# Kernel optimization log

Measured on AMD Instinct MI355X. Metric: run time of the kernel, lower is better.

The kernel has to match this reference:

```python
import jax, jax.numpy as jnp
import numpy as np

N_NODES = 100000
N_PER_GRAPH = 200
N_GRAPHS = N_NODES // N_PER_GRAPH
N_EDGES = 400000
F_IN = 37
H = 128          # node_hidden == transformer_hidden == fc_hidden
HEADS = 8
K_SEEDS = 75     # ceil(0.25 * 300) -> PyG GMT defaults


def _lin(key, out_d, in_d):
    kw, kb = jax.random.split(key)
    w = jax.random.normal(kw, (out_d, in_d), jnp.float32) * float(1.0 / np.sqrt(in_d))
    b = jax.random.normal(kb, (out_d,), jnp.float32) * 0.02
    return w, b


def gcn_layer(x, W, b, src, dst, n):
    # PyG GCNConv with add_self_loops and symmetric deg^-1/2 normalization
    h = x @ W.T                                   # [n, out]
    deg = jnp.ones((n,), h.dtype).at[dst].add(1.0)   # in-degree + self loop
    dinv = jax.lax.rsqrt(deg)
    msg = h[src] * (dinv[src] * dinv[dst])[:, None]  # gather + edge normalize
    agg = jnp.zeros_like(h).at[dst].add(msg)         # scatter-add
    agg = agg + h * (dinv * dinv)[:, None]           # self-loop message
    return agg + b


def attn_block(Q, K, V, fo_W, fo_b):
    # MAB core of GMT: multi-head attention (scaled by sqrt(dim_V)) + rFF residual
    B, nq, d = Q.shape
    dh = d // HEADS
    Qh = Q.reshape(B, nq, HEADS, dh)
    Kh = K.reshape(B, K.shape[1], HEADS, dh)
    Vh = V.reshape(B, V.shape[1], HEADS, dh)
    scores = jnp.einsum('bqhd,bkhd->bhqk', Qh, Kh) / jnp.sqrt(jnp.asarray(d, Q.dtype))
    A = jax.nn.softmax(scores, axis=-1)
    O = jnp.einsum('bhqk,bkhd->bqhd', A, Vh).reshape(B, nq, d)
    out = Q + O
    return out + jax.nn.relu(out @ fo_W.T + fo_b)


def setup_inputs() -> dict:
    key = jax.random.key(0)
    k = iter(jax.random.split(key, 64))
    inp = {}
    inp['herg_em'] = jax.random.normal(next(k), (1, 1280), jnp.float32)
    inp['x'] = jax.random.normal(next(k), (N_NODES, F_IN), jnp.float32)
    inp['edge_attr'] = jax.random.normal(next(k), (N_EDGES, 4), jnp.float32)
    inp['mol_rep'] = jax.random.normal(next(k), (N_GRAPHS, 11), jnp.float32)
    for i, in_d in enumerate([F_IN, H, H, H]):
        inp[f'conv_W{i}'], inp[f'conv_b{i}'] = _lin(next(k), H, in_d)
    inp['lin1_W'], inp['lin1_b'] = _lin(next(k), H, H)
    inp['lin2_W'], inp['lin2_b'] = _lin(next(k), H, H)
    inp['S1'] = jax.random.normal(next(k), (1, K_SEEDS, H), jnp.float32) * 0.1
    for p in ['pma1', 'sab', 'pma2']:
        for nm in ['fq', 'k', 'v', 'fo']:
            inp[f'{p}_{nm}_W'], inp[f'{p}_{nm}_b'] = _lin(next(k), H, H)
    inp['S2'] = jax.random.normal(next(k), (1, 1, H), jnp.float32) * 0.1
    inp['herg_lin_W'], inp['herg_lin_b'] = _lin(next(k), H, 1280)
    inp['herg_out_W'], inp['herg_out_b'] = _lin(next(k), H, 2 * H)
    inp['fc0_W'], inp['fc0_b'] = _lin(next(k), H, H)
    inp['sig_W'], inp['sig_b'] = _lin(next(k), 1, H)
    inp['edge_index'] = jax.random.randint(next(k), (2, N_EDGES), 0, N_NODES, dtype=jnp.int32)
    inp['batch'] = jnp.arange(N_NODES, dtype=jnp.int32) // N_PER_GRAPH
    return inp


def reference(herg_em, x, edge_attr, mol_rep,
              conv_W0, conv_b0, conv_W1, conv_b1, conv_W2, conv_b2, conv_W3, conv_b3,
              lin1_W, lin1_b, lin2_W, lin2_b,
              S1, pma1_fq_W, pma1_fq_b, pma1_k_W, pma1_k_b, pma1_v_W, pma1_v_b, pma1_fo_W, pma1_fo_b,
              sab_fq_W, sab_fq_b, sab_k_W, sab_k_b, sab_v_W, sab_v_b, sab_fo_W, sab_fo_b,
              S2, pma2_fq_W, pma2_fq_b, pma2_k_W, pma2_k_b, pma2_v_W, pma2_v_b, pma2_fo_W, pma2_fo_b,
              herg_lin_W, herg_lin_b, herg_out_W, herg_out_b,
              fc0_W, fc0_b, sig_W, sig_b,
              edge_index, batch):
    src, dst = edge_index[0], edge_index[1]
    n = x.shape[0]

    # stacked GCNConv + ReLU
    h = jax.nn.relu(gcn_layer(x, conv_W0, conv_b0, src, dst, n))
    for W, b in ((conv_W1, conv_b1), (conv_W2, conv_b2), (conv_W3, conv_b3)):
        h = jax.nn.relu(gcn_layer(h, W, b, src, dst, n))

    # GraphMultisetTransformer: lin1 -> GMPool_G -> SelfAtt -> GMPool_I -> lin2
    hx = h @ lin1_W.T + lin1_b                     # [N, H]
    B = N_GRAPHS

    # GMPool_G: seeds attend to GCNConv-projected keys/values (dense per graph)
    Q = jnp.broadcast_to(S1, (B, K_SEEDS, H)) @ pma1_fq_W.T + pma1_fq_b
    K = gcn_layer(hx, pma1_k_W, pma1_k_b, src, dst, n).reshape(B, N_PER_GRAPH, H)
    V = gcn_layer(hx, pma1_v_W, pma1_v_b, src, dst, n).reshape(B, N_PER_GRAPH, H)
    xb = attn_block(Q, K, V, pma1_fo_W, pma1_fo_b)     # [B, 75, H]

    # SelfAtt (SAB)
    Q = xb @ sab_fq_W.T + sab_fq_b
    K = xb @ sab_k_W.T + sab_k_b
    V = xb @ sab_v_W.T + sab_v_b
    xb = attn_block(Q, K, V, sab_fo_W, sab_fo_b)       # [B, 75, H]

    # GMPool_I: single seed, Linear keys/values
    Q = jnp.broadcast_to(S2, (B, 1, H)) @ pma2_fq_W.T + pma2_fq_b
    K = xb @ pma2_k_W.T + pma2_k_b
    V = xb @ pma2_v_W.T + pma2_v_b
    xb = attn_block(Q, K, V, pma2_fo_W, pma2_fo_b)     # [B, 1, H]

    out = xb[:, 0, :] @ lin2_W.T + lin2_b              # [B, H]

    # hERG branch
    herg = jax.nn.relu(herg_em @ herg_lin_W.T + herg_lin_b)   # [1, 128]
    herg = jnp.broadcast_to(herg, (B, herg.shape[1]))
    out = jnp.concatenate([out, herg], axis=1)                 # [B, 256]
    out = jax.nn.relu(out @ herg_out_W.T + herg_out_b)
    out = jax.nn.relu(out @ fc0_W.T + fc0_b)                   # dropout = identity (eval)
    return jax.nn.sigmoid(out @ sig_W.T + sig_b)               # [B, 1]
```

## Files before the change

### kernel.cpp

```cpp
#include <hip/hip_runtime.h>
#include <hip/hip_bf16.h>

typedef unsigned short ushort_t;
typedef unsigned int uint_t;
typedef __attribute__((ext_vector_type(8))) short short8;
typedef __attribute__((ext_vector_type(4))) float float4v;

static constexpr int NN  = 100000;
static constexpr int NE  = 400000;
static constexpr int NB  = 500;
static constexpr int NS  = 75;
static constexpr int H   = 128;
static constexpr float SCALE = 0.08838834764831845f;

union U32 { uint_t u; float f; };
__device__ __forceinline__ float bf2f(ushort_t b){ U32 t; t.u = ((uint_t)b) << 16; return t.f; }
__device__ __forceinline__ ushort_t f2bf(float f){
    U32 t; t.f = f;
    uint_t r = t.u + 0x7fffu + ((t.u >> 16) & 1u);
    return (ushort_t)(r >> 16);
}
__device__ __forceinline__ void fma8(float* a, uint4 u, float c){
    a[0] += c * bf2f((ushort_t)(u.x & 0xffff)); a[1] += c * bf2f((ushort_t)(u.x >> 16));
    a[2] += c * bf2f((ushort_t)(u.y & 0xffff)); a[3] += c * bf2f((ushort_t)(u.y >> 16));
    a[4] += c * bf2f((ushort_t)(u.z & 0xffff)); a[5] += c * bf2f((ushort_t)(u.z >> 16));
    a[6] += c * bf2f((ushort_t)(u.w & 0xffff)); a[7] += c * bf2f((ushort_t)(u.w >> 16));
}

__global__ void k_hist(int* counts, const int* __restrict__ dst, int e){
    int i = blockIdx.x*256 + threadIdx.x;
    if (i < e) atomicAdd(&counts[dst[i]], 1);
}
__global__ __launch_bounds__(256) void k_scan1(const int* __restrict__ counts,
    int* __restrict__ row_start, int* __restrict__ blockSums,
    float* __restrict__ dinv, float* __restrict__ selfc, int n){
    __shared__ int s[256];
    int t = threadIdx.x, i = blockIdx.x*256 + t;
    int v = (i < n) ? counts[i] : 0;
    s[t] = v; __syncthreads();
    #pragma unroll
    for (int off = 1; off < 256; off <<= 1){
        int add = (t >= off) ? s[t-off] : 0;
        __syncthreads();
        s[t] += add;
        __syncthreads();
    }
    if (i < n){
        row_start[i] = s[t] - v;
        float r = rsqrtf(1.f + (float)v);
        dinv[i] = r; selfc[i] = r*r;
    }
    if (t == 255) blockSums[blockIdx.x] = s[255];
}
__global__ __launch_bounds__(512) void k_scan2(const int* __restrict__ blockSums,
    int* __restrict__ blockOff, int nb){
    __shared__ int s[512];
    int t = threadIdx.x;
    int v = (t < nb) ? blockSums[t] : 0;
    s[t] = v; __syncthreads();
    #pragma unroll
    for (int off = 1; off < 512; off <<= 1){
        int add = (t >= off) ? s[t-off] : 0;
        __syncthreads();
        s[t] += add;
        __syncthreads();
    }
    blockOff[t] = s[t] - v;
}
__global__ void k_scan3(int* __restrict__ row_start, int* __restrict__ cursor,
                        const int* __restrict__ blockOff, int n, int total){
    int i = blockIdx.x*256 + threadIdx.x;
    if (i < n){
        int v = row_start[i] + blockOff[i >> 8];
        row_start[i] = v; cursor[i] = v;
    }
    if (i == 0) row_start[n] = total;
}
__global__ void k_fillcsr(const int* __restrict__ src, const int* __restrict__ dst,
    const float* __restrict__ dinv, int* cursor,
    int* __restrict__ srcs_s, float* __restrict__ ce_s, int e){
    int i = blockIdx.x*256 + threadIdx.x;
    if (i < e){
        int d = dst[i], s = src[i];
        int p = atomicAdd(&cursor[d], 1);
        srcs_s[p] = s;
        ce_s[p] = dinv[s] * dinv[d];
    }
}

struct CvtArgs { const float* w[17]; const float* w0; const float* s1; const float* s2; const float* x37; };
static constexpr int CVT_W   = 17*16384;
static constexpr int CVT_W0  = 8192;
static constexpr int CVT_S1  = 9600;
static constexpr int CVT_S2  = 128;
static constexpr int CVT_X   = NN*64;
__global__ void k_cvt_all(CvtArgs a, ushort_t* __restrict__ wbf, ushort_t* __restrict__ w0bf,
                          ushort_t* __restrict__ s1bf, ushort_t* __restrict__ s2bf,
                          ushort_t* __restrict__ xb64, int* __restrict__ counts){
    int i = blockIdx.x*256 + threadIdx.x;
    if (i < NN) counts[i] = 0;
    if (i < CVT_W){ int idx = i >> 14, off = i & 16383; wbf[i] = f2bf(a.w[idx][off]); return; }
    i -= CVT_W;
    if (i < CVT_W0){ int r = i >> 6, c = i & 63; w0bf[i] = (c < 37) ? f2bf(a.w0[r*37 + c]) : (ushort_t)0; return; }
    i -= CVT_W0;
    if (i < CVT_S1){ s1bf[i] = f2bf(a.s1[i]); return; }
    i -= CVT_S1;
    if (i < CVT_S2){ s2bf[i] = f2bf(a.s2[i]); return; }
    i -= CVT_S2;
    if (i < CVT_X){ int r = i >> 6, c = i & 63; xb64[i] = (c < 37) ? f2bf(a.x37[(size_t)r*37 + c]) : (ushort_t)0; return; }
}

__global__ __launch_bounds__(256) void k_seedq(
    const ushort_t* __restrict__ s1bf, const ushort_t* __restrict__ s2bf,
    const ushort_t* __restrict__ W1, const float* __restrict__ bias1,
    const ushort_t* __restrict__ W2q, const float* __restrict__ bias2,
    ushort_t* __restrict__ q0, ushort_t* __restrict__ q2,
    const float* __restrict__ hem, const float* __restrict__ hlW,
    const float* __restrict__ hlb, float* __restrict__ hergv)
{
    int blk = blockIdx.x;
    int tid  = threadIdx.x;
    if (blk == 3){
        __shared__ float e[1280];
        for (int i = tid; i < 1280; i += 256) e[i] = hem[i];
        __syncthreads();
        if (tid < 128){
            float acc = 0.f;
            for (int k = 0; k < 1280; ++k) acc += e[k] * hlW[(size_t)tid*1280 + k];
            hergv[tid] = fmaxf(acc + hlb[tid], 0.f);
        }
        return;
    }
    const ushort_t* x = (blk < 2) ? s1bf : s2bf;
    const ushort_t* W = (blk < 2) ? W1 : W2q;
    const float* bias = (blk < 2) ? bias1 : bias2;
    ushort_t* out = (blk < 2) ? q0 : q2;
    int M = (blk < 2) ? NS : 1;
    int base = (blk < 2) ? blk*64 : 0;
    int wid  = tid >> 6;
    int lane = tid & 63;
    int l15  = lane & 15, quad = lane >> 4;
    int row0 = base + wid*16;
    int ar   = row0 + l15; if (ar > M-1) ar = M-1;
    const short* xr = (const short*)(x + (size_t)ar*H) + quad*8;
    float4v acc[8];
    #pragma unroll
    for (int i = 0; i < 8; ++i) acc[i] = (float4v)0.f;
    #pragma unroll
    for (int kc = 0; kc < 4; ++kc){
        short8 a = *(const short8*)(xr + kc*32);
        #pragma unroll
        for (int nt = 0; nt < 8; ++nt){
            short8 b = *(const short8*)((const short*)(W + (size_t)(nt*16 + l15)*H) + kc*32 + quad*8);
            acc[nt] = __builtin_amdgcn_mfma_f32_16x16x32_bf16(a, b, acc[nt], 0, 0, 0);
        }
    }
    #pragma unroll
    for (int nt = 0; nt < 8; ++nt){
        int c = nt*16 + l15;
        float bv = bias[c];
        #pragma unroll
        for (int reg = 0; reg < 4; ++reg){
            int r = row0 + quad*4 + reg;
            if (r >= M) continue;
            out[(size_t)r*H + c] = f2bf(acc[nt][reg] + bv);
        }
    }
}

template<int NOUT, int RELU, int STAGE2, int MINW>
__global__ __launch_bounds__(256, MINW) void k_conv_fused3(
    const ushort_t* __restrict__ x,
    const int* __restrict__ row_st, const int* __restrict__ srcs,
    const float* __restrict__ ces, const float* __restrict__ selfc,
    const ushort_t* __restrict__ W, const float* __restrict__ bias0,
    const float* __restrict__ bias1,
    const ushort_t* __restrict__ W2, const float* __restrict__ bias2,
    ushort_t* __restrict__ out0, ushort_t* __restrict__ out1)
{
    __shared__ ushort_t As[32][136];
    __shared__ ushort_t Bs[(NOUT==16)?32:1][(NOUT==16)?136:1];
    const int tid = threadIdx.x;
    const int node = tid >> 3, qq = tid & 7;
    const int g = blockIdx.x*32 + node;
    float acc[16];
    #pragma unroll
    for (int i = 0; i < 16; ++i) acc[i] = 0.f;
    if (g < NN){
        const uint4* xr = (const uint4*)(x + (size_t)g*H + qq*16);
        float sc = selfc[g];
        uint4 u0 = xr[0], u1 = xr[1];
        fma8(acc+0, u0, sc); fma8(acc+8, u1, sc);
        int e = row_st[g], e1 = row_st[g+1];
        int sA = 0, sB = 0; float cA = 0.f, cB = 0.f;
        if (e < e1){ sA = srcs[e]; cA = ces[e]; }
        if (e + 1 < e1){ sB = srcs[e+1]; cB = ces[e+1]; }
        while (e + 2 <= e1){
            int sA2 = 0, sB2 = 0; float cA2 = 0.f, cB2 = 0.f;
            if (e + 2 < e1){ sA2 = srcs[e+2]; cA2 = ces[e+2]; }
            if (e + 3 < e1){ sB2 = srcs[e+3]; cB2 = ces[e+3]; }
            const uint4* pa = (const uint4*)(x + (size_t)sA*H + qq*16);
            const uint4* pb = (const uint4*)(x + (size_t)sB*H + qq*16);
            uint4 a0 = pa[0], a1 = pa[1];
            uint4 c0 = pb[0], c1 = pb[1];
            fma8(acc+0, a0, cA); fma8(acc+8, a1, cA);
            fma8(acc+0, c0, cB); fma8(acc+8, c1, cB);
            sA = sA2; sB = sB2; cA = cA2; cB = cB2;
            e += 2;
        }
        if (e < e1){
            const uint4* pa = (const uint4*)(x + (size_t)sA*H + qq*16);
            uint4 a0 = pa[0], a1 = pa[1];
            fma8(acc+0, a0, cA); fma8(acc+8, a1, cA);
        }
    }
    {
        uint_t* dst = (uint_t*)&As[node][qq*16];
        #pragma unroll
        for (int i = 0; i < 8; ++i)
            dst[i] = (uint_t)f2bf(acc[2*i]) | ((uint_t)f2bf(acc[2*i+1]) << 16);
    }
    __syncthreads();
    const int w = tid >> 6, lane = tid & 63, l15 = lane & 15, quad = lane >> 4;
    const int rt = w & 1;
    constexpr int NT = NOUT/2;
    const int ct0 = (w >> 1) * NT;
    float4v o[NT];
    #pragma unroll
    for (int t = 0; t < NT; ++t) o[t] = (float4v)0.f;
    #pragma unroll
    for (int kc = 0; kc < 4; ++kc){
        short8 a = *(const short8*)(&As[rt*16 + l15][kc*32 + quad*8]);
        #pragma unroll
        for (int t = 0; t < NT; ++t){
            short8 bfr = *(const short8*)(W + (size_t)((ct0 + t)*16 + l15)*H + kc*32 + quad*8);
            o[t] = __builtin_amdgcn_mfma_f32_16x16x32_bf16(a, bfr, o[t], 0, 0, 0);
        }
    }
    __syncthreads();
    #pragma unroll
    for (int t = 0; t < NT; ++t){
        int cg = (ct0 + t)*16 + l15;
        #pragma unroll
        for (int r = 0; r < 4; ++r){
            float v;
            if (NOUT == 8 || cg < 128){
                v = o[t][r] + bias0[cg];
                if (RELU) v = fmaxf(v, 0.f);
                As[rt*16 + quad*4 + r][cg] = f2bf(v);
            } else {
                v = o[t][r] + bias1[cg - 128];
                if (RELU) v = fmaxf(v, 0.f);
                Bs[rt*16 + quad*4 + r][cg - 128] = f2bf(v);
            }
        }
    }
    __syncthreads();
    if (STAGE2){
        float4v o2[4];
        #pragma unroll
        for (int t = 0; t < 4; ++t) o2[t] = (float4v)0.f;
        const int ct2 = (w >> 1) * 4;
        #pragma unroll
        for (int kc = 0; kc < 4; ++kc){
            short8 a = *(const short8*)(&As[rt*16 + l15][kc*32 + quad*8]);
            #pragma unroll
            for (int t = 0; t < 4; ++t){
                short8 bfr = *(const short8*)(W2 + (size_t)((ct2 + t)*16 + l15)*H + kc*32 + quad*8);
                o2[t] = __builtin_amdgcn_mfma_f32_16x16x32_bf16(a, bfr, o2[t], 0, 0, 0);
            }
        }
        __syncthreads();
        #pragma unroll
        for (int t = 0; t < 4; ++t){
            int cg = (ct2 + t)*16 + l15;
            #pragma unroll
            for (int r = 0; r < 4; ++r)
                As[rt*16 + quad*4 + r][cg] = f2bf(o2[t][r] + bias2[cg]);
        }
        __syncthreads();
    }
    if (g < NN){
        if (NOUT == 16){
            size_t kb = ((size_t)(qq >> 1)*NN + (size_t)g)*32 + (size_t)(qq & 1)*16;
            ((uint4*)(out0 + kb))[0] = *(const uint4*)&As[node][qq*16];
            ((uint4*)(out0 + kb))[1] = *(const uint4*)&As[node][qq*16 + 8];
            ((uint4*)(out1 + kb))[0] = *(const uint4*)&Bs[node][qq*16];
            ((uint4*)(out1 + kb))[1] = *(const uint4*)&Bs[node][qq*16 + 8];
        } else {
            uint4* op = (uint4*)(out0 + (size_t)g*H + qq*16);
            const uint4* sp = (const uint4*)&As[node][qq*16];
            op[0] = sp[0]; op[1] = sp[1];
        }
    }
}

__global__ __launch_bounds__(256, 8) void k_conv0b(
    const ushort_t* __restrict__ x,
    const int* __restrict__ row_st, const int* __restrict__ srcs,
    const float* __restrict__ ces, const float* __restrict__ selfc,
    const ushort_t* __restrict__ W,
    const float* __restrict__ bias,
    ushort_t* __restrict__ out)
{
    __shared__ ushort_t As[32][136];
    const int tid = threadIdx.x;
    const int node = tid >> 3, qq = tid & 7;
    const int g = blockIdx.x*32 + node;
    float acc[8];
    #pragma unroll
    for (int i = 0; i < 8; ++i) acc[i] = 0.f;
    if (g < NN){
        const uint4* xr = (const uint4*)(x + (size_t)g*64 + qq*8);
        float sc = selfc[g];
        fma8(acc, xr[0], sc);
        int e = row_st[g], e1 = row_st[g+1];
        int sA = 0, sB = 0; float cA = 0.f, cB = 0.f;
        if (e < e1){ sA = srcs[e]; cA = ces[e]; }
        if (e + 1 < e1){ sB = srcs[e+1]; cB = ces[e+1]; }
        while (e + 2 <= e1){
            int sA2 = 0, sB2 = 0; float cA2 = 0.f, cB2 = 0.f;
            if (e + 2 < e1){ sA2 = srcs[e+2]; cA2 = ces[e+2]; }
            if (e + 3 < e1){ sB2 = srcs[e+3]; cB2 = ces[e+3]; }
            uint4 a0 = *(const uint4*)(x + (size_t)sA*64 + qq*8);
            uint4 c0 = *(const uint4*)(x + (size_t)sB*64 + qq*8);
            fma8(acc, a0, cA);
            fma8(acc, c0, cB);
            sA = sA2; sB = sB2; cA = cA2; cB = cB2;
            e += 2;
        }
        if (e < e1){
            uint4 a0 = *(const uint4*)(x + (size_t)sA*64 + qq*8);
            fma8(acc, a0, cA);
        }
    }
    {
        uint_t* dst = (uint_t*)&As[node][qq*8];
        #pragma unroll
        for (int i = 0; i < 4; ++i)
            dst[i] = (uint_t)f2bf(acc[2*i]) | ((uint_t)f2bf(acc[2*i+1]) << 16);
    }
    __syncthreads();
    const int w = tid >> 6, lane = tid & 63, l15 = lane & 15, quad = lane >> 4;
    const int rt = w & 1;
    const int ct0 = (w >> 1) * 4;
    float4v o[4];
    #pragma unroll
    for (int t = 0; t < 4; ++t) o[t] = (float4v)0.f;
    #pragma unroll
    for (int kc = 0; kc < 2; ++kc){
        short8 a = *(const short8*)(&As[rt*16 + l15][kc*32 + quad*8]);
        #pragma unroll
        for (int t = 0; t < 4; ++t){
            short8 bfr = *(const short8*)(W + (size_t)((ct0 + t)*16 + l15)*64 + kc*32 + quad*8);
            o[t] = __builtin_amdgcn_mfma_f32_16x16x32_bf16(a, bfr, o[t], 0, 0, 0);
        }
    }
    __syncthreads();
    #pragma unroll
    for (int t = 0; t < 4; ++t){
        int cg = (ct0 + t)*16 + l15;
        #pragma unroll
        for (int r = 0; r < 4; ++r)
            As[rt*16 + quad*4 + r][cg] = f2bf(fmaxf(o[t][r] + bias[cg], 0.f));
    }
    __syncthreads();
    if (g < NN){
        uint4* op = (uint4*)(out + (size_t)g*H + qq*16);
        const uint4* sp = (const uint4*)&As[node][qq*16];
        op[0] = sp[0]; op[1] = sp[1];
    }
}

template<int NK, int HM>
__global__ __launch_bounds__(256) void k_attn_mfma(
    const ushort_t* __restrict__ Q, int qbs,
    const ushort_t* __restrict__ K, const ushort_t* __restrict__ V,
    ushort_t* __restrict__ out, int nq)
{
    constexpr int NKT = (NK + 15) / 16;
    constexpr int NKC = (NK + 31) / 32;
    __shared__ ushort_t Ks[2][208][24];
    __shared__ ushort_t Vs[2][16][232];
    __shared__ ushort_t Ps[4][16][232];
    int b = blockIdx.x >> 2, hp = blockIdx.x & 3;
    int h0 = hp*2;
    int tid = threadIdx.x;
    {
        uint_t* p = (uint_t*)&Ps[0][0][0];
        for (int i = tid; i < 4*16*232/2; i += 256) p[i] = 0;
    }
    const ushort_t* Kb = HM ? (K + ((size_t)hp*NB + b)*NK*32)
                            : (K + (size_t)b*NK*H + h0*16);
    for (int idx = tid; idx < NK*8; idx += 256){
        int key = idx >> 3, p = idx & 7;
        int hh = p >> 2, dl = (p & 3)*4;
        const uint_t* src = HM ? (const uint_t*)(Kb + (size_t)key*32 + hh*16 + dl)
                               : (const uint_t*)(Kb + (size_t)key*H + hh*16 + dl);
        uint_t* d = (uint_t*)&Ks[hh][key][dl];
        d[0] = src[0]; d[1] = src[1];
    }
    const ushort_t* Vb = HM ? (V + ((size_t)hp*NB + b)*NK*32)
                            : (V + (size_t)b*NK*H + h0*16);
    for (int idx = tid; idx < NK*8; idx += 256){
        int key = idx >> 3, p = idx & 7;
        int hh = p >> 2, dl = (p & 3)*4;
        const ushort_t* src = HM ? (Vb + (size_t)key*32 + hh*16 + dl)
                                 : (Vb + (size_t)key*H + hh*16 + dl);
        Vs[hh][dl+0][key] = src[0];
        Vs[hh][dl+1][key] = src[1];
        Vs[hh][dl+2][key] = src[2];
        Vs[hh][dl+3][key] = src[3];
    }
    for (int idx = tid; idx < 2*16*(232-NK); idx += 256){
        int key = NK + idx % (232-NK), r = idx / (232-NK);
        Vs[r>>4][r&15][key] = 0;
    }
    __syncthreads();

    int w = tid >> 6, lane = tid & 63;
    int hh = w >> 1, half = w & 1;
    int h = h0 + hh;
    int l15 = lane & 15, quad = lane >> 4;
    bool klow = (quad < 2);
    int nqt = (nq + 15) >> 4;
    int split = (nqt + 1) >> 1;
    int qt0 = half ? split : 0;
    int qt1 = half ? nqt : split;
    for (int qt = qt0; qt < qt1; ++qt){
        int qr = qt*16 + l15; if (qr > nq-1) qr = nq-1;
        short8 av = *(const short8*)(Q + (size_t)b*qbs + (size_t)qr*H + h*16 + (quad & 1)*8);
        short8 zero8 = (short8)0;
        short8 afrag = klow ? av : zero8;
        float4v s[NKT];
        #pragma unroll
        for (int kt = 0; kt < NKT; ++kt){
            short8 bv = *(const short8*)(&Ks[hh][kt*16 + l15][(quad & 1)*8]);
            short8 bfrag = klow ? bv : zero8;
            s[kt] = __builtin_amdgcn_mfma_f32_16x16x32_bf16(afrag, bfrag, (float4v)0.f, 0, 0, 0);
        }
        float mx[4] = {-1e30f, -1e30f, -1e30f, -1e30f};
        #pragma unroll
        for (int kt = 0; kt < NKT; ++kt){
            if (kt*16 + l15 >= NK){ s[kt][0]=-1e30f; s[kt][1]=-1e30f; s[kt][2]=-1e30f; s[kt][3]=-1e30f; }
            #pragma unroll
            for (int r = 0; r < 4; ++r) mx[r] = fmaxf(mx[r], s[kt][r]);
        }
        #pragma unroll
        for (int off = 1; off < 16; off <<= 1){
            #pragma unroll
            for (int r = 0; r < 4; ++r) mx[r] = fmaxf(mx[r], __shfl_xor(mx[r], off));
        }
        float sum[4] = {0.f, 0.f, 0.f, 0.f};
        #pragma unroll
        for (int kt = 0; kt < NKT; ++kt){
            #pragma unroll
            for (int r = 0; r < 4; ++r){
                float e = __expf((s[kt][r] - mx[r]) * SCALE);
                sum[r] += e;
                Ps[w][quad*4 + r][kt*16 + l15] = f2bf(e);
            }
        }
        #pragma unroll
        for (int off = 1; off < 16; off <<= 1){
            #pragma unroll
            for (int r = 0; r < 4; ++r) sum[r] += __shfl_xor(sum[r], off);
        }
        float4v o = (float4v)0.f;
        #pragma unroll
        for (int kc = 0; kc < NKC; ++kc){
            short8 pa = *(const short8*)(&Ps[w][l15][kc*32 + quad*8]);
            short8 vb = *(const short8*)(&Vs[hh][l15][kc*32 + quad*8]);
            o = __builtin_amdgcn_mfma_f32_16x16x32_bf16(pa, vb, o, 0, 0, 0);
        }
        #pragma unroll
        for (int r = 0; r < 4; ++r){
            int row = qt*16 + quad*4 + r;
            if (row < nq){
                float qv = bf2f(Q[(size_t)b*qbs + (size_t)row*H + h*16 + l15]);
                out[((size_t)b*nq + row)*H + h*16 + l15] = f2bf(qv + o[r] / sum[r]);
            }
        }
    }
}

struct TailArgs {
    const ushort_t* xA; const ushort_t* q2;
    const ushort_t* p1foW; const float* p1fob;
    const ushort_t* sfqW;  const float* sfqb;
    const ushort_t* skW;   const float* skb;
    const ushort_t* svW;   const float* svb;
    const ushort_t* sfoW;  const float* sfob;
    const ushort_t* p2kW;  const float* p2kb;
    const ushort_t* p2vW;  const float* p2vb;
    const ushort_t* p2foW; const float* p2fob;
    const ushort_t* lin2W; const float* lin2b;
    const float* hergv;
    const float* hoW; const float* hob;
    const float* fcW; const float* fcb;
    const float* sW;  const float* sb;
    float* outp;
};

__global__ __launch_bounds__(256, 1) void k_graph_tail(TailArgs a){
    __shared__ ushort_t bufQ[80*136];
    __shared__ ushort_t bufX[80*136];
    __shared__ ushort_t bufK[80*136];
    __shared__ ushort_t vt[8*16*104];
    __shared__ ushort_t ps[4*16*104];
    const int b = blockIdx.x, tid = threadIdx.x;
    const int w = tid >> 6, lane = tid & 63, l15 = lane & 15, quad = lane >> 4;

    for (int i = tid; i < 8*16*104/2; i += 256) ((uint_t*)vt)[i] = 0u;
    for (int i = tid; i < 4*16*104/2; i += 256) ((uint_t*)ps)[i] = 0u;
    {
        const ushort_t* xg = a.xA + (size_t)b*NS*H;
        for (int i = tid; i < NS*16; i += 256){
            int row = i >> 4, q = i & 15;
            *(uint4*)(bufQ + row*136 + q*8) = *(const uint4*)(xg + (size_t)row*H + q*8);
        }
    }
    __syncthreads();

    for (int job = w; job < 40; job += 4){
        int rt = job >> 3, ct = job & 7;
        float4v o = (float4v)0.f;
        #pragma unroll
        for (int kc = 0; kc < 4; ++kc){
            short8 av = *(const short8*)(bufQ + (rt*16 + l15)*136 + kc*32 + quad*8);
            short8 bv = *(const short8*)((const short*)(a.p1foW + (size_t)(ct*16 + l15)*H) + kc*32 + quad*8);
            o = __builtin_amdgcn_mfma_f32_16x16x32_bf16(av, bv, o, 0, 0, 0);
        }
        int c = ct*16 + l15; float bb = a.p1fob[c];
        #pragma unroll
        for (int r = 0; r < 4; ++r){
            int row = rt*16 + quad*4 + r;
            bufX[row*136 + c] = f2bf(fmaxf(o[r] + bb, 0.f) + bf2f(bufQ[row*136 + c]));
        }
    }
    __syncthreads();

    for (int job = w; job < 40; job += 4){
        int rt = job >> 3, ct = job & 7;
        float4v o = (float4v)0.f;
        #pragma unroll
        for (int kc = 0; kc < 4; ++kc){
            short8 av = *(const short8*)(bufX + (rt*16 + l15)*136 + kc*32 + quad*8);
            short8 bv = *(const short8*)((const short*)(a.sfqW + (size_t)(ct*16 + l15)*H) + kc*32 + quad*8);
            o = __builtin_amdgcn_mfma_f32_16x16x32_bf16(av, bv, o, 0, 0, 0);
        }
        int c = ct*16 + l15; float bb = a.sfqb[c];
        #pragma unroll
        for (int r = 0; r < 4; ++r)
            bufQ[(rt*16 + quad*4 + r)*136 + c] = f2bf(o[r] + bb);
    }
    for (int job = w; job < 40; job += 4){
        int rt = job >> 3, ct = job & 7;
        float4v o = (float4v)0.f;
        #pragma unroll
        for (int kc = 0; kc < 4; ++kc){
            short8 av = *(const short8*)(bufX + (rt*16 + l15)*136 + kc*32 + quad*8);
            short8 bv = *(const short8*)((const short*)(a.skW + (size_t)(ct*16 + l15)*H) + kc*32 + quad*8);
            o = __builtin_amdgcn_mfma_f32_16x16x32_bf16(av, bv, o, 0, 0, 0);
        }
        int c = ct*16 + l15; float bb = a.skb[c];
        #pragma unroll
        for (int r = 0; r < 4; ++r)
            bufK[(rt*16 + quad*4 + r)*136 + c] = f2bf(o[r] + bb);
    }
    for (int job = w; job < 40; job += 4){
        int rt = job >> 3, ct = job & 7;
        float4v o = (float4v)0.f;
        #pragma unroll
        for (int kc = 0; kc < 4; ++kc){
            short8 av = *(const short8*)(bufX + (rt*16 + l15)*136 + kc*32 + quad*8);
            short8 bv = *(const short8*)((const short*)(a.svW + (size_t)(ct*16 + l15)*H) + kc*32 + quad*8);
            o = __builtin_amdgcn_mfma_f32_16x16x32_bf16(av, bv, o, 0, 0, 0);
        }
        int c = ct*16 + l15; float bb = a.svb[c];
        #pragma unroll
        for (int r = 0; r < 4; ++r){
            int key = rt*16 + quad*4 + r;
            if (key < NS) vt[c*104 + key] = f2bf(o[r] + bb);
        }
    }
    __syncthreads();

    {
        short8 zero8 = (short8)0;
        bool klow = (quad < 2);
        for (int hh = 0; hh < 2; ++hh){
            int h = w*2 + hh;
            for (int qt = 0; qt < 5; ++qt){
                short8 av = *(const short8*)(bufQ + (qt*16 + l15)*136 + h*16 + (quad & 1)*8);
                short8 afrag = klow ? av : zero8;
                float4v s[5];
                #pragma unroll
                for (int kt = 0; kt < 5; ++kt){
                    short8 bv = *(const short8*)(bufK + (kt*16 + l15)*136 + h*16 + (quad & 1)*8);
                    short8 bfrag = klow ? bv : zero8;
                    s[kt] = __builtin_amdgcn_mfma_f32_16x16x32_bf16(afrag, bfrag, (float4v)0.f, 0, 0, 0);
                }
                float mx[4] = {-1e30f, -1e30f, -1e30f, -1e30f};
                #pragma unroll
                for (int kt = 0; kt < 5; ++kt){
                    if (kt*16 + l15 >= NS){ s[kt][0]=-1e30f; s[kt][1]=-1e30f; s[kt][2]=-1e30f; s[kt][3]=-1e30f; }
                    #pragma unroll
                    for (int r = 0; r < 4; ++r) mx[r] = fmaxf(mx[r], s[kt][r]);
                }
                #pragma unroll
                for (int off = 1; off < 16; off <<= 1){
                    #pragma unroll
                    for (int r = 0; r < 4; ++r) mx[r] = fmaxf(mx[r], __shfl_xor(mx[r], off));
                }
                float sum[4] = {0.f, 0.f, 0.f, 0.f};
                #pragma unroll
                for (int kt = 0; kt < 5; ++kt){
                    #pragma unroll
                    for (int r = 0; r < 4; ++r){
                        float e = __expf((s[kt][r] - mx[r]) * SCALE);
                        sum[r] += e;
                        ps[w*1664 + (quad*4 + r)*104 + kt*16 + l15] = f2bf(e);
                    }
                }
                #pragma unroll
                for (int off = 1; off < 16; off <<= 1){
                    #pragma unroll
                    for (int r = 0; r < 4; ++r) sum[r] += __shfl_xor(sum[r], off);
                }
                float4v o = (float4v)0.f;
                #pragma unroll
                for (int kc = 0; kc < 3; ++kc){
                    short8 pa = *(const short8*)(ps + w*1664 + l15*104 + kc*32 + quad*8);
                    short8 vb = *(const short8*)(vt + (h*16 + l15)*104 + kc*32 + quad*8);
                    o = __builtin_amdgcn_mfma_f32_16x16x32_bf16(pa, vb, o, 0, 0, 0);
                }
                #pragma unroll
                for (int r = 0; r < 4; ++r){
                    int row = qt*16 + quad*4 + r;
                    if (row < NS){
                        float qv = bf2f(bufQ[row*136 + h*16 + l15]);
                        bufQ[row*136 + h*16 + l15] = f2bf(qv + o[r] / sum[r]);
                    }
                }
            }
        }
    }
    __syncthreads();

    for (int job = w; job < 40; job += 4){
        int rt = job >> 3, ct = job & 7;
        float4v o = (float4v)0.f;
        #pragma unroll
        for (int kc = 0; kc < 4; ++kc){
            short8 av = *(const short8*)(bufQ + (rt*16 + l15)*136 + kc*32 + quad*8);
            short8 bv = *(const short8*)((const short*)(a.sfoW + (size_t)(ct*16 + l15)*H) + kc*32 + quad*8);
            o = __builtin_amdgcn_mfma_f32_16x16x32_bf16(av, bv, o, 0, 0, 0);
        }
        int c = ct*16 + l15; float bb = a.sfob[c];
        #pragma unroll
        for (int r = 0; r < 4; ++r){
            int row = rt*16 + quad*4 + r;
            bufX[row*136 + c] = f2bf(fmaxf(o[r] + bb, 0.f) + bf2f(bufQ[row*136 + c]));
        }
    }
    __syncthreads();

    for (int job = w; job < 40; job += 4){
        int rt = job >> 3, ct = job & 7;
        float4v o = (float4v)0.f;
        #pragma unroll
        for (int kc = 0; kc < 4; ++kc){
            short8 av = *(const short8*)(bufX + (rt*16 + l15)*136 + kc*32 + quad*8);
            short8 bv = *(const short8*)((const short*)(a.p2kW + (size_t)(ct*16 + l15)*H) + kc*32 + quad*8);
            o = __builtin_amdgcn_mfma_f32_16x16x32_bf16(av, bv, o, 0, 0, 0);
        }
        int c = ct*16 + l15; float bb = a.p2kb[c];
        #pragma unroll
        for (int r = 0; r < 4; ++r)
            bufK[(rt*16 + quad*4 + r)*136 + c] = f2bf(o[r] + bb);
    }
    for (int job = w; job < 40; job += 4){
        int rt = job >> 3, ct = job & 7;
        float4v o = (float4v)0.f;
        #pragma unroll
        for (int kc = 0; kc < 4; ++kc){
            short8 av = *(const short8*)(bufX + (rt*16 + l15)*136 + kc*32 + quad*8);
            short8 bv = *(const short8*)((const short*)(a.p2vW + (size_t)(ct*16 + l15)*H) + kc*32 + quad*8);
            o = __builtin_amdgcn_mfma_f32_16x16x32_bf16(av, bv, o, 0, 0, 0);
        }
        int c = ct*16 + l15; float bb = a.p2vb[c];
        #pragma unroll
        for (int r = 0; r < 4; ++r)
            bufQ[(rt*16 + quad*4 + r)*136 + c] = f2bf(o[r] + bb);
    }
    __syncthreads();

    {
        int t = tid;
        char* sb8 = (char*)ps;
        float* sc       = (float*)sb8;
        float* sumh     = (float*)(sb8 + 2432);
        ushort_t* xa    = (ushort_t*)(sb8 + 2464);
        ushort_t* xb3   = (ushort_t*)(sb8 + 2720);
        float* tt       = (float*)(sb8 + 2976);
        float* v256     = (float*)(sb8 + 3488);
        float* red      = (float*)(sb8 + 4512);
        {
            int h = t >> 5, l32 = t & 31;
            const ushort_t* qr = a.q2 + h*16;
            for (int k = l32; k < NS; k += 32){
                float s = 0.f;
                #pragma unroll
                for (int d = 0; d < 16; ++d) s += bf2f(qr[d]) * bf2f(bufK[k*136 + h*16 + d]);
                sc[h*76 + k] = s;
            }
        }
        __syncthreads();
        if (t < 128){
            int hh = t >> 4, i = t & 15;
            float mx = -1e30f;
            for (int k = i; k < NS; k += 16) mx = fmaxf(mx, sc[hh*76 + k]);
            #pragma unroll
            for (int off = 1; off < 16; off <<= 1) mx = fmaxf(mx, __shfl_xor(mx, off));
            float sm = 0.f;
            for (int k = i; k < NS; k += 16){
                float e = __expf((sc[hh*76 + k] - mx) * SCALE);
                sc[hh*76 + k] = e;
                sm += e;
            }
            #pragma unroll
            for (int off = 1; off < 16; off <<= 1) sm += __shfl_xor(sm, off);
            if (i == 0) sumh[hh] = sm;
        }
        __syncthreads();
        if (t < 128){
            int hh = t >> 4;
            float o = 0.f;
            for (int k = 0; k < NS; ++k) o += sc[hh*76 + k] * bf2f(bufQ[k*136 + t]);
            xa[t] = f2bf(bf2f(a.q2[t]) + o / sumh[hh]);
        }
        __syncthreads();
        if (t < 128){
            float acc = 0.f;
            const ushort_t* wr = a.p2foW + (size_t)t*H;
            for (int k = 0; k < H; ++k) acc += bf2f(xa[k]) * bf2f(wr[k]);
            xb3[t] = f2bf(fmaxf(acc + a.p2fob[t], 0.f) + bf2f(xa[t]));
        }
        __syncthreads();
        if (t < 128){
            float acc = 0.f;
            const ushort_t* wr = a.lin2W + (size_t)t*H;
            for (int k = 0; k < H; ++k) acc += bf2f(xb3[k]) * bf2f(wr[k]);
            v256[t] = acc + a.lin2b[t];
            v256[128 + t] = a.hergv[t];
        }
        __syncthreads();
        if (t < 128){
            float acc = 0.f;
            const float* wr = a.hoW + (size_t)t*256;
            for (int k = 0; k < 256; ++k) acc += v256[k] * wr[k];
            tt[t] = fmaxf(acc + a.hob[t], 0.f);
        }
        __syncthreads();
        if (t < 128){
            float acc = 0.f;
            const float* wr = a.fcW + (size_t)t*128;
            for (int k = 0; k < 128; ++k) acc += tt[k] * wr[k];
            float uv = fmaxf(acc + a.fcb[t], 0.f);
            red[t] = uv * a.sW[t];
        }
        __syncthreads();
        for (int s = 64; s > 0; s >>= 1){
            if (t < s) red[t] += red[t + s];
            __syncthreads();
        }
        if (t == 0){
            float logit = red[0] + a.sb[0];
            a.outp[b] = 1.f / (1.f + expf(-logit));
        }
    }
}

extern "C" void kernel_launch(void* const* d_in, const int* in_sizes, int n_in,
                              void* d_out, int out_size, void* d_ws, size_t ws_size,
                              hipStream_t stream)
{
    (void)in_sizes; (void)n_in; (void)out_size; (void)ws_size;
    const float* herg_em = (const float*)d_in[0];
    const float* x_in    = (const float*)d_in[1];
    const float* convW[4] = {(const float*)d_in[4], (const float*)d_in[6], (const float*)d_in[8], (const float*)d_in[10]};
    const float* convB[4] = {(const float*)d_in[5], (const float*)d_in[7], (const float*)d_in[9], (const float*)d_in[11]};
    const float* lin1W = (const float*)d_in[12]; const float* lin1b = (const float*)d_in[13];
    const float* lin2W = (const float*)d_in[14]; const float* lin2b = (const float*)d_in[15];
    const float* S1    = (const float*)d_in[16];
    const float* p1fqW = (const float*)d_in[17]; const float* p1fqb = (const float*)d_in[18];
    const float* p1kW  = (const float*)d_in[19]; const float* p1kb  = (const float*)d_in[20];
    const float* p1vW  = (const float*)d_in[21]; const float* p1vb  = (const float*)d_in[22];
    const float* p1foW = (const float*)d_in[23]; const float* p1fob = (const float*)d_in[24];
    const float* sfqW  = (const float*)d_in[25]; const float* sfqb  = (const float*)d_in[26];
    const float* skW   = (const float*)d_in[27]; const float* skb   = (const float*)d_in[28];
    const float* svW   = (const float*)d_in[29]; const float* svb   = (const float*)d_in[30];
    const float* sfoW  = (const float*)d_in[31]; const float* sfob  = (const float*)d_in[32];
    const float* p2fqW = (const float*)d_in[33]; const float* p2fqb = (const float*)d_in[34];
    const float* p2kW  = (const float*)d_in[35]; const float* p2kb  = (const float*)d_in[36];
    const float* p2vW  = (const float*)d_in[37]; const float* p2vb  = (const float*)d_in[38];
    const float* p2foW = (const float*)d_in[39]; const float* p2fob = (const float*)d_in[40];
    const float* S2    = (const float*)d_in[41];
    const float* hlW   = (const float*)d_in[42]; const float* hlb   = (const float*)d_in[43];
    const float* hoW   = (const float*)d_in[44]; const float* hob   = (const float*)d_in[45];
    const float* fcW   = (const float*)d_in[46]; const float* fcb   = (const float*)d_in[47];
    const float* sW    = (const float*)d_in[48]; const float* sb    = (const float*)d_in[49];
    const int*  ei    = (const int*)d_in[50];
    const int*  esrc  = ei;
    const int*  edst  = ei + NE;
    float* outp = (float*)d_out;

    char* WS = (char*)d_ws;
    int*   counts = (int*)(WS + 0);
    int*   cursor = (int*)(WS + 400384);
    int*   row_st = (int*)(WS + 800768);
    int*   bSums  = (int*)(WS + 1201152);
    int*   bOff   = (int*)(WS + 1203200);
    float* dinv   = (float*)(WS + 1205248);
    float* selfc  = (float*)(WS + 1605632);
    int*   srcs_s = (int*)(WS + 2005632);
    float* ce_s   = (float*)(WS + 3605632);
    ushort_t* wbf = (ushort_t*)(WS + 5205632);
    ushort_t* w0bf= (ushort_t*)(WS + 5762688);
    ushort_t* s1bf= (ushort_t*)(WS + 5779072);
    ushort_t* s2bf= (ushort_t*)(WS + 5798272);
    ushort_t* q0  = (ushort_t*)(WS + 5798528);
    ushort_t* q2  = (ushort_t*)(WS + 5817728);
    float* hergv  = (float*)(WS + 5817984);
    ushort_t* xb64= (ushort_t*)(WS + 6074496);
    ushort_t* b0  = (ushort_t*)(WS + 18874496);
    ushort_t* b1  = (ushort_t*)(WS + 44474496);
    ushort_t* b2  = (ushort_t*)(WS + 70074496);
    ushort_t* xA  = (ushort_t*)(WS + 95674496);

    const int gN   = (NN + 255)/256;
    const int gE   = (NE + 255)/256;
    const int gC   = (NN + 31)/32;

    CvtArgs ca;
    ca.w[0]=convW[1]; ca.w[1]=convW[2]; ca.w[2]=convW[3]; ca.w[3]=lin1W; ca.w[4]=lin2W;
    ca.w[5]=p1kW; ca.w[6]=p1vW; ca.w[7]=p1foW;
    ca.w[8]=sfqW; ca.w[9]=skW; ca.w[10]=svW; ca.w[11]=sfoW;
    ca.w[12]=p2kW; ca.w[13]=p2vW; ca.w[14]=p2foW; ca.w[15]=p1fqW; ca.w[16]=p2fqW;
    ca.w0 = convW[0]; ca.s1 = S1; ca.s2 = S2; ca.x37 = x_in;
    const int cvtTotal = CVT_W + CVT_W0 + CVT_S1 + CVT_S2 + CVT_X;
    k_cvt_all<<<(cvtTotal + 255)/256, 256, 0, stream>>>(ca, wbf, w0bf, s1bf, s2bf, xb64, counts);

    k_hist  <<<gE, 256, 0, stream>>>(counts, edst, NE);
    k_scan1 <<<gN, 256, 0, stream>>>(counts, row_st, bSums, dinv, selfc, NN);
    k_scan2 <<<1, 512, 0, stream>>>(bSums, bOff, gN);
    k_scan3 <<<gN, 256, 0, stream>>>(row_st, cursor, bOff, NN, NE);
    k_fillcsr<<<gE, 256, 0, stream>>>(esrc, edst, dinv, cursor, srcs_s, ce_s, NE);

    k_seedq<<<4, 256, 0, stream>>>(s1bf, s2bf, wbf + (size_t)15*16384, p1fqb,
                                   wbf + (size_t)16*16384, p2fqb, q0, q2,
                                   herg_em, hlW, hlb, hergv);

    k_conv0b<<<gC, 256, 0, stream>>>(xb64, row_st, srcs_s, ce_s, selfc, w0bf, convB[0], b0);
    k_conv_fused3<8,1,0,8><<<gC, 256, 0, stream>>>(b0, row_st, srcs_s, ce_s, selfc,
        wbf + (size_t)0*16384, convB[1], nullptr, nullptr, nullptr, b1, nullptr);
    k_conv_fused3<8,1,0,8><<<gC, 256, 0, stream>>>(b1, row_st, srcs_s, ce_s, selfc,
        wbf + (size_t)1*16384, convB[2], nullptr, nullptr, nullptr, b0, nullptr);
    k_conv_fused3<8,1,1,8><<<gC, 256, 0, stream>>>(b0, row_st, srcs_s, ce_s, selfc,
        wbf + (size_t)2*16384, convB[3], nullptr, wbf + (size_t)3*16384, lin1b, b1, nullptr);
    k_conv_fused3<16,0,0,4><<<gC, 256, 0, stream>>>(b1, row_st, srcs_s, ce_s, selfc,
        wbf + (size_t)5*16384, p1kb, p1vb, nullptr, nullptr, b2, b0);
    k_attn_mfma<200,1><<<NB*4, 256, 0, stream>>>(q0, 0, b2, b0, xA, NS);

    TailArgs ta;
    ta.xA = xA; ta.q2 = q2;
    ta.p1foW = wbf + (size_t)7*16384;  ta.p1fob = p1fob;
    ta.sfqW  = wbf + (size_t)8*16384;  ta.sfqb  = sfqb;
    ta.skW   = wbf + (size_t)9*16384;  ta.skb   = skb;
    ta.svW   = wbf + (size_t)10*16384; ta.svb   = svb;
    ta.sfoW  = wbf + (size_t)11*16384; ta.sfob  = sfob;
    ta.p2kW  = wbf + (size_t)12*16384; ta.p2kb  = p2kb;
    ta.p2vW  = wbf + (size_t)13*16384; ta.p2vb  = p2vb;
    ta.p2foW = wbf + (size_t)14*16384; ta.p2fob = p2fob;
    ta.lin2W = wbf + (size_t)4*16384;  ta.lin2b = lin2b;
    ta.hergv = hergv;
    ta.hoW = hoW; ta.hob = hob;
    ta.fcW = fcW; ta.fcb = fcb;
    ta.sW = sW; ta.sb = sb;
    ta.outp = outp;
    k_graph_tail<<<NB, 256, 0, stream>>>(ta);
}
```

Measured before the change: 731.7 us.

## Shrink tail-kernel LDS footprint to allow two blocks per CU

```diff
diff --git a/kernel.cpp b/kernel.cpp
--- a/kernel.cpp
+++ b/kernel.cpp
@@ -502,22 +502,49 @@
     float* outp;
 };
 
-__global__ __launch_bounds__(256, 1) void k_graph_tail(TailArgs a){
-    __shared__ ushort_t bufQ[80*136];
-    __shared__ ushort_t bufX[80*136];
-    __shared__ ushort_t bufK[80*136];
-    __shared__ ushort_t vt[8*16*104];
-    __shared__ ushort_t ps[4*16*104];
+__global__ __launch_bounds__(256, 2) void k_graph_tail(TailArgs a){
+    __shared__ ushort_t bufA[83*136];
+    __shared__ ushort_t bufB[80*136];
+    __shared__ ushort_t bufC[80*136];
+    __shared__ ushort_t vt4[64*104];
     const int b = blockIdx.x, tid = threadIdx.x;
     const int w = tid >> 6, lane = tid & 63, l15 = lane & 15, quad = lane >> 4;
-
-    for (int i = tid; i < 8*16*104/2; i += 256) ((uint_t*)vt)[i] = 0u;
-    for (int i = tid; i < 4*16*104/2; i += 256) ((uint_t*)ps)[i] = 0u;
+    ushort_t* psw = (w == 0) ? bufA + 10200 :
+                    (w == 1) ? bufA + 10712 :
+                    (w == 2) ? bufB + 10200 : bufC + 10200;
+
+    for (int i = tid; i < 64*104/2; i += 256) ((uint_t*)vt4)[i] = 0u;
     {
         const ushort_t* xg = a.xA + (size_t)b*NS*H;
         for (int i = tid; i < NS*16; i += 256){
             int row = i >> 4, q = i & 15;
-            *(uint4*)(bufQ + row*136 + q*8) = *(const uint4*)(xg + (size_t)row*H + q*8);
+            *(uint4*)(bufA + row*136 + q*8) = *(const uint4*)(xg + (size_t)row*H + q*8);
+        }
+    }
+    __syncthreads();
+
+    for (int rt = w; rt < 5; rt += 4){
+        float4v o[8];
+        #pragma unroll
+        for (int i = 0; i < 8; ++i) o[i] = (float4v)0.f;
+        #pragma unroll
+        for (int kc = 0; kc < 4; ++kc){
+            short8 av = *(const short8*)(bufA + (rt*16 + l15)*136 + kc*32 + quad*8);
+            #pragma unroll
+            for (int ct = 0; ct < 8; ++ct){
+                short8 bv = *(const short8*)((const short*)(a.p1foW + (size_t)(ct*16 + l15)*H) + kc*32 + quad*8);
+                o[ct] = __builtin_amdgcn_mfma_f32_16x16x32_bf16(av, bv, o[ct], 0, 0, 0);
+            }
+        }
+        #pragma unroll
+        for (int ct = 0; ct < 8; ++ct){
+            int c = ct*16 + l15; float bb = a.p1fob[c];
+            #pragma unroll
+            for (int r = 0; r < 4; ++r){
+                int row = rt*16 + quad*4 + r;
+                float res = bf2f(bufA[row*136 + c]);
+                bufA[row*136 + c] = f2bf(fmaxf(o[ct][r] + bb, 0.f) + res);
+            }
         }
     }
     __syncthreads();
@@ -527,77 +554,62 @@
         float4v o = (float4v)0.f;
         #pragma unroll
         for (int kc = 0; kc < 4; ++kc){
-            short8 av = *(const short8*)(bufQ + (rt*16 + l15)*136 + kc*32 + quad*8);
-            short8 bv = *(const short8*)((const short*)(a.p1foW + (size_t)(ct*16 + l15)*H) + kc*32 + quad*8);
+            short8 av = *(const short8*)(bufA + (rt*16 + l15)*136 + kc*32 + quad*8);
+            short8 bv = *(const short8*)((const short*)(a.sfqW + (size_t)(ct*16 + l15)*H) + kc*32 + quad*8);
             o = __builtin_amdgcn_mfma_f32_16x16x32_bf16(av, bv, o, 0, 0, 0);
         }
-        int c = ct*16 + l15; float bb = a.p1fob[c];
-        #pragma unroll
-        for (int r = 0; r < 4; ++r){
-            int row = rt*16 + quad*4 + r;
-            bufX[row*136 + c] = f2bf(fmaxf(o[r] + bb, 0.f) + bf2f(bufQ[row*136 + c]));
-        }
-    }
-    __syncthreads();
-
+        int c = ct*16 + l15; float bb = a.sfqb[c];
+        #pragma unroll
+        for (int r = 0; r < 4; ++r)
+            bufB[(rt*16 + quad*4 + r)*136 + c] = f2bf(o[r] + bb);
+    }
     for (int job = w; job < 40; job += 4){
         int rt = job >> 3, ct = job & 7;
         float4v o = (float4v)0.f;
         #pragma unroll
         for (int kc = 0; kc < 4; ++kc){
-            short8 av = *(const short8*)(bufX + (rt*16 + l15)*136 + kc*32 + quad*8);
-            short8 bv = *(const short8*)((const short*)(a.sfqW + (size_t)(ct*16 + l15)*H) + kc*32 + quad*8);
-            o = __builtin_amdgcn_mfma_f32_16x16x32_bf16(av, bv, o, 0, 0, 0);
-        }
-        int c = ct*16 + l15; float bb = a.sfqb[c];
-        #pragma unroll
-        for (int r = 0; r < 4; ++r)
-            bufQ[(rt*16 + quad*4 + r)*136 + c] = f2bf(o[r] + bb);
-    }
-    for (int job = w; job < 40; job += 4){
-        int rt = job >> 3, ct = job & 7;
-        float4v o = (float4v)0.f;
-        #pragma unroll
-        for (int kc = 0; kc < 4; ++kc){
-            short8 av = *(const short8*)(bufX + (rt*16 + l15)*136 + kc*32 + quad*8);
+            short8 av = *(const short8*)(bufA + (rt*16 + l15)*136 + kc*32 + quad*8);
             short8 bv = *(const short8*)((const short*)(a.skW + (size_t)(ct*16 + l15)*H) + kc*32 + quad*8);
             o = __builtin_amdgcn_mfma_f32_16x16x32_bf16(av, bv, o, 0, 0, 0);
         }
         int c = ct*16 + l15; float bb = a.skb[c];
         #pragma unroll
         for (int r = 0; r < 4; ++r)
-            bufK[(rt*16 + quad*4 + r)*136 + c] = f2bf(o[r] + bb);
-    }
-    for (int job = w; job < 40; job += 4){
-        int rt = job >> 3, ct = job & 7;
-        float4v o = (float4v)0.f;
-        #pragma unroll
-        for (int kc = 0; kc < 4; ++kc){
-            short8 av = *(const short8*)(bufX + (rt*16 + l15)*136 + kc*32 + quad*8);
-            short8 bv = *(const short8*)((const short*)(a.svW + (size_t)(ct*16 + l15)*H) + kc*32 + quad*8);
-            o = __builtin_amdgcn_mfma_f32_16x16x32_bf16(av, bv, o, 0, 0, 0);
-        }
-        int c = ct*16 + l15; float bb = a.svb[c];
-        #pragma unroll
-        for (int r = 0; r < 4; ++r){
-            int key = rt*16 + quad*4 + r;
-            if (key < NS) vt[c*104 + key] = f2bf(o[r] + bb);
-        }
-    }
-    __syncthreads();
-
-    {
-        short8 zero8 = (short8)0;
-        bool klow = (quad < 2);
-        for (int hh = 0; hh < 2; ++hh){
-            int h = w*2 + hh;
+            bufC[(rt*16 + quad*4 + r)*136 + c] = f2bf(o[r] + bb);
+    }
+    __syncthreads();
+
+    for (int pass = 0; pass < 2; ++pass){
+        int hbase = pass*4;
+        for (int job = w; job < 20; job += 4){
+            int rt = job >> 2, ctl = job & 3;
+            int ct = hbase + ctl;
+            float4v o = (float4v)0.f;
+            #pragma unroll
+            for (int kc = 0; kc < 4; ++kc){
+                short8 av = *(const short8*)(bufA + (rt*16 + l15)*136 + kc*32 + quad*8);
+                short8 bv = *(const short8*)((const short*)(a.svW + (size_t)(ct*16 + l15)*H) + kc*32 + quad*8);
+                o = __builtin_amdgcn_mfma_f32_16x16x32_bf16(av, bv, o, 0, 0, 0);
+            }
+            int c = ct*16 + l15; float bb = a.svb[c];
+            #pragma unroll
+            for (int r = 0; r < 4; ++r){
+                int key = rt*16 + quad*4 + r;
+                if (key < NS) vt4[(ctl*16 + l15)*104 + key] = f2bf(o[r] + bb);
+            }
+        }
+        __syncthreads();
+        {
+            int hl = w, h = hbase + w;
+            short8 zero8 = (short8)0;
+            bool klow = (quad < 2);
             for (int qt = 0; qt < 5; ++qt){
-                short8 av = *(const short8*)(bufQ + (qt*16 + l15)*136 + h*16 + (quad & 1)*8);
+                short8 av = *(const short8*)(bufB + (qt*16 + l15)*136 + h*16 + (quad & 1)*8);
                 short8 afrag = klow ? av : zero8;
                 float4v s[5];
                 #pragma unroll
                 for (int kt = 0; kt < 5; ++kt){
-                    short8 bv = *(const short8*)(bufK + (kt*16 + l15)*136 + h*16 + (quad & 1)*8);
+                    short8 bv = *(const short8*)(bufC + (kt*16 + l15)*136 + h*16 + (quad & 1)*8);
                     short8 bfrag = klow ? bv : zero8;
                     s[kt] = __builtin_amdgcn_mfma_f32_16x16x32_bf16(afrag, bfrag, (float4v)0.f, 0, 0, 0);
                 }
@@ -614,46 +626,47 @@
                     for (int r = 0; r < 4; ++r) mx[r] = fmaxf(mx[r], __shfl_xor(mx[r], off));
                 }
                 float sum[4] = {0.f, 0.f, 0.f, 0.f};
+                float4v o = (float4v)0.f;
                 #pragma unroll
-                for (int kt = 0; kt < 5; ++kt){
+                for (int kc = 0; kc < 3; ++kc){
                     #pragma unroll
-                    for (int r = 0; r < 4; ++r){
-                        float e = __expf((s[kt][r] - mx[r]) * SCALE);
-                        sum[r] += e;
-                        ps[w*1664 + (quad*4 + r)*104 + kt*16 + l15] = f2bf(e);
+                    for (int t2 = 0; t2 < 2; ++t2){
+                        int kt = kc*2 + t2;
+                        #pragma unroll
+                        for (int r = 0; r < 4; ++r){
+                            float e = 0.f;
+                            if (kt < 5){ e = __expf((s[kt][r] - mx[r]) * SCALE); sum[r] += e; }
+                            psw[(quad*4 + r)*32 + t2*16 + l15] = f2bf(e);
+                        }
                     }
+                    short8 pa = *(const short8*)(psw + l15*32 + quad*8);
+                    short8 vb = *(const short8*)(vt4 + (hl*16 + l15)*104 + kc*32 + quad*8);
+                    o = __builtin_amdgcn_mfma_f32_16x16x32_bf16(pa, vb, o, 0, 0, 0);
                 }
                 #pragma unroll
                 for (int off = 1; off < 16; off <<= 1){
                     #pragma unroll
                     for (int r = 0; r < 4; ++r) sum[r] += __shfl_xor(sum[r], off);
                 }
-                float4v o = (float4v)0.f;
-                #pragma unroll
-                for (int kc = 0; kc < 3; ++kc){
-                    short8 pa = *(const short8*)(ps + w*1664 + l15*104 + kc*32 + quad*8);
-                    short8 vb = *(const short8*)(vt + (h*16 + l15)*104 + kc*32 + quad*8);
-                    o = __builtin_amdgcn_mfma_f32_16x16x32_bf16(pa, vb, o, 0, 0, 0);
-                }
                 #pragma unroll
                 for (int r = 0; r < 4; ++r){
                     int row = qt*16 + quad*4 + r;
                     if (row < NS){
-                        float qv = bf2f(bufQ[row*136 + h*16 + l15]);
-                        bufQ[row*136 + h*16 + l15] = f2bf(qv + o[r] / sum[r]);
+                        float qv = bf2f(bufB[row*136 + h*16 + l15]);
+                        bufB[row*136 + h*16 + l15] = f2bf(qv + o[r] / sum[r]);
                     }
                 }
             }
         }
-    }
-    __syncthreads();
+        __syncthreads();
+    }
 
     for (int job = w; job < 40; job += 4){
         int rt = job >> 3, ct = job & 7;
         float4v o = (float4v)0.f;
         #pragma unroll
         for (int kc = 0; kc < 4; ++kc){
-            short8 av = *(const short8*)(bufQ + (rt*16 + l15)*136 + kc*32 + quad*8);
+            short8 av = *(const short8*)(bufB + (rt*16 + l15)*136 + kc*32 + quad*8);
             short8 bv = *(const short8*)((const short*)(a.sfoW + (size_t)(ct*16 + l15)*H) + kc*32 + quad*8);
             o = __builtin_amdgcn_mfma_f32_16x16x32_bf16(av, bv, o, 0, 0, 0);
         }
@@ -661,7 +674,7 @@
         #pragma unroll
         for (int r = 0; r < 4; ++r){
             int row = rt*16 + quad*4 + r;
-            bufX[row*136 + c] = f2bf(fmaxf(o[r] + bb, 0.f) + bf2f(bufQ[row*136 + c]));
+            bufA[row*136 + c] = f2bf(fmaxf(o[r] + bb, 0.f) + bf2f(bufB[row*136 + c]));
         }
     }
     __syncthreads();
@@ -671,34 +684,34 @@
         float4v o = (float4v)0.f;
         #pragma unroll
         for (int kc = 0; kc < 4; ++kc){
-            short8 av = *(const short8*)(bufX + (rt*16 + l15)*136 + kc*32 + quad*8);
+            short8 av = *(const short8*)(bufA + (rt*16 + l15)*136 + kc*32 + quad*8);
             short8 bv = *(const short8*)((const short*)(a.p2kW + (size_t)(ct*16 + l15)*H) + kc*32 + quad*8);
             o = __builtin_amdgcn_mfma_f32_16x16x32_bf16(av, bv, o, 0, 0, 0);
         }
         int c = ct*16 + l15; float bb = a.p2kb[c];
         #pragma unroll
         for (int r = 0; r < 4; ++r)
-            bufK[(rt*16 + quad*4 + r)*136 + c] = f2bf(o[r] + bb);
+            bufC[(rt*16 + quad*4 + r)*136 + c] = f2bf(o[r] + bb);
     }
     for (int job = w; job < 40; job += 4){
         int rt = job >> 3, ct = job & 7;
         float4v o = (float4v)0.f;
         #pragma unroll
         for (int kc = 0; kc < 4; ++kc){
-            short8 av = *(const short8*)(bufX + (rt*16 + l15)*136 + kc*32 + quad*8);
+            short8 av = *(const short8*)(bufA + (rt*16 + l15)*136 + kc*32 + quad*8);
             short8 bv = *(const short8*)((const short*)(a.p2vW + (size_t)(ct*16 + l15)*H) + kc*32 + quad*8);
             o = __builtin_amdgcn_mfma_f32_16x16x32_bf16(av, bv, o, 0, 0, 0);
         }
         int c = ct*16 + l15; float bb = a.p2vb[c];
         #pragma unroll
         for (int r = 0; r < 4; ++r)
-            bufQ[(rt*16 + quad*4 + r)*136 + c] = f2bf(o[r] + bb);
+            bufB[(rt*16 + quad*4 + r)*136 + c] = f2bf(o[r] + bb);
     }
     __syncthreads();
 
     {
         int t = tid;
-        char* sb8 = (char*)ps;
+        char* sb8 = (char*)bufA;
         float* sc       = (float*)sb8;
         float* sumh     = (float*)(sb8 + 2432);
         ushort_t* xa    = (ushort_t*)(sb8 + 2464);
@@ -712,7 +725,7 @@
             for (int k = l32; k < NS; k += 32){
                 float s = 0.f;
                 #pragma unroll
-                for (int d = 0; d < 16; ++d) s += bf2f(qr[d]) * bf2f(bufK[k*136 + h*16 + d]);
+                for (int d = 0; d < 16; ++d) s += bf2f(qr[d]) * bf2f(bufC[k*136 + h*16 + d]);
                 sc[h*76 + k] = s;
             }
         }
@@ -737,7 +750,7 @@
         if (t < 128){
             int hh = t >> 4;
             float o = 0.f;
-            for (int k = 0; k < NS; ++k) o += sc[hh*76 + k] * bf2f(bufQ[k*136 + t]);
+            for (int k = 0; k < NS; ++k) o += sc[hh*76 + k] * bf2f(bufB[k*136 + t]);
             xa[t] = f2bf(bf2f(a.q2[t]) + o / sumh[hh]);
         }
         __syncthreads();
```

Measured after the change: 693.6 us. -5.2%, faster.
